# Kernel optimization log

Measured on AMD Instinct MI355X. Metric: run time of the kernel, lower is better.

The kernel has to match this reference:

```python
import jax, jax.numpy as jnp
import numpy as np

B, LAT, H, N, NL = 16, 64, 128, 256, 3
STATS = 7
IU, JU = np.triu_indices(N, 1)  # P = N*(N-1)/2 upper-triangular pairs


def _ln(x, g, b):
    m = jnp.mean(x, axis=-1, keepdims=True)
    v = jnp.var(x, axis=-1, keepdims=True)
    return (x - m) / jnp.sqrt(v + 1e-5) * g + b


def setup_inputs() -> dict:
    key = jax.random.key(0)
    ks = jax.random.split(key, 16)
    s = 0.02  # xavier-ish small gain per _init_weights
    L = NL - 1
    return {
        "x": jax.random.normal(ks[0], (B, LAT), jnp.float32),
        "stats": jax.random.normal(ks[1], (B, STATS), jnp.float32),
        # input_proj: Linear(LAT+7, 2H) + LN(2H)
        "ip_w": jax.random.normal(ks[2], (LAT + STATS, 2 * H)) * s,
        "ip_b": jnp.zeros((2 * H,)),
        "ip_ln_g": jnp.ones((2 * H,)),
        "ip_ln_b": jnp.zeros((2 * H,)),
        # dim_reduce: Linear(2H, H) + LN(H)
        "dr_w": jax.random.normal(ks[3], (2 * H, H)) * s,
        "dr_b": jnp.zeros((H,)),
        "dr_ln_g": jnp.ones((H,)),
        "dr_ln_b": jnp.zeros((H,)),
        # residual blocks (NL-1 of them), proj is Identity since in==out
        "res_lin1_w": jax.random.normal(ks[4], (L, H, H)) * s,
        "res_lin1_b": jnp.zeros((L, H)),
        "res_lin2_w": jax.random.normal(ks[5], (L, H, H)) * s,
        "res_lin2_b": jnp.zeros((L, H)),
        "res_n1_g": jnp.ones((L, H)),
        "res_n1_b": jnp.zeros((L, H)),
        "res_n2_g": jnp.ones((L, H)),
        "res_n2_b": jnp.zeros((L, H)),
        # attention: Linear(H, 1)
        "attn_w": jax.random.normal(ks[6], (H, 1)) * s,
        "attn_b": jnp.zeros((1,)),
        # edge_mlp: Linear(2H, H) + LN(H) + Linear(H, 2)
        "e1_w": jax.random.normal(ks[7], (2 * H, H)) * s,
        "e1_b": jnp.zeros((H,)),
        "e_ln_g": jnp.ones((H,)),
        "e_ln_b": jnp.zeros((H,)),
        "e2_w": jax.random.normal(ks[8], (H, 2)) * s,
        "e2_b": jnp.zeros((2,)),
        "temperature": jnp.ones((1,)) * 0.5,
    }


def reference(x, stats, ip_w, ip_b, ip_ln_g, ip_ln_b, dr_w, dr_b, dr_ln_g,
              dr_ln_b, res_lin1_w, res_lin1_b, res_lin2_w, res_lin2_b,
              res_n1_g, res_n1_b, res_n2_g, res_n2_b, attn_w, attn_b,
              e1_w, e1_b, e_ln_g, e_ln_b, e2_w, e2_b, temperature):
    # concat latent + stats, broadcast to every node: [B, N, LAT+7]
    z = jnp.concatenate([x, stats], axis=-1)
    z = jnp.broadcast_to(z[:, None, :], (B, N, LAT + STATS))
    # input_proj (dropout is identity in eval)
    h = _ln(jax.nn.relu(z @ ip_w + ip_b), ip_ln_g, ip_ln_b)
    # dim_reduce
    h = _ln(jax.nn.relu(h @ dr_w + dr_b), dr_ln_g, dr_ln_b)
    # residual blocks: h = h + 0.1 * block(h); block(h) = mlp(h) + h
    for l in range(res_lin1_w.shape[0]):
        r = _ln(h, res_n1_g[l], res_n1_b[l])
        r = jax.nn.relu(r @ res_lin1_w[l] + res_lin1_b[l])
        r = _ln(r, res_n2_g[l], res_n2_b[l])
        r = r @ res_lin2_w[l] + res_lin2_b[l]
        h = h + 0.1 * (r + h)
    # simple attention over node axis
    w = jax.nn.softmax(h @ attn_w + attn_b, axis=1)  # [B, N, 1]
    h = h * w
    # batched edge MLP over all i<j pairs: [B, P, 2H]
    edge_in = jnp.concatenate([h[:, IU], h[:, JU]], axis=-1)
    e = _ln(jax.nn.relu(edge_in @ e1_w + e1_b), e_ln_g, e_ln_b)
    logits = e @ e2_w + e2_b  # [B, P, 2]
    # gumbel-softmax (hard, straight-through), fixed key for determinism
    temp = jnp.clip(temperature, 0.1, 2.0)
    u = jax.random.uniform(jax.random.key(42), logits.shape,
                           minval=1e-9, maxval=1.0)
    gumbel = -jnp.log(-jnp.log(u))
    y = jax.nn.softmax((logits + gumbel) / temp, axis=-1)
    y_hard = jax.nn.one_hot(jnp.argmax(y, axis=-1), 2, dtype=y.dtype)
    y = y_hard + y - jax.lax.stop_gradient(y)
    xe = y[..., 0]  # [B, P]
    # scatter into upper triangle, symmetrize
    adj = jnp.zeros((B, N, N), dtype=xe.dtype).at[:, IU, JU].set(xe)
    return adj + jnp.swapaxes(adj, 1, 2)
```

## Files before the change

kernel.cpp:

```cpp
#include <hip/hip_runtime.h>
#include <stdint.h>
#include <math.h>

#define BN 16
#define LATN 64
#define STATSN 7
#define ZN 71
#define HN 128
#define H2N 256
#define NNODE 256
#define NPAIR 32640
#define NQ 522240
#define NT 1024

#define BARRIER() asm volatile("s_waitcnt lgkmcnt(0)\n\ts_barrier" ::: "memory")

__device__ __forceinline__ void tf2x32(uint32_t x0, uint32_t x1,
                                       uint32_t& o0, uint32_t& o1) {
    const uint32_t ks0 = 0u, ks1 = 42u, ks2 = 0x1BD11BF0u;
    x0 += ks0; x1 += ks1;
#define TFRND(r) { x0 += x1; x1 = (x1 << (r)) | (x1 >> (32 - (r))); x1 ^= x0; }
    TFRND(13) TFRND(15) TFRND(26) TFRND(6)
    x0 += ks1; x1 += ks2 + 1u;
    TFRND(17) TFRND(29) TFRND(16) TFRND(24)
    x0 += ks2; x1 += ks0 + 2u;
    TFRND(13) TFRND(15) TFRND(26) TFRND(6)
    x0 += ks0; x1 += ks1 + 3u;
    TFRND(17) TFRND(29) TFRND(16) TFRND(24)
    x0 += ks1; x1 += ks2 + 4u;
    TFRND(13) TFRND(15) TFRND(26) TFRND(6)
    x0 += ks2; x1 += ks0 + 5u;
#undef TFRND
    o0 = x0; o1 = x1;
}

__device__ __forceinline__ uint32_t bits_partitionable(uint32_t m) {
    uint32_t o0, o1;
    tf2x32(0u, m, o0, o1);
    return o0 ^ o1;
}

__device__ __forceinline__ float bits_to_u(uint32_t w) {
    float f = __uint_as_float((w >> 9) | 0x3f800000u) - 1.0f;
    const float mn = 1e-9f;
    return fmaxf(mn, f * (1.0f - mn) + mn);
}

template<int CTRL>
__device__ __forceinline__ double dppd(double x) {
    int lo = __double2loint(x), hi = __double2hiint(x);
    lo = __builtin_amdgcn_update_dpp(0, lo, CTRL, 0xF, 0xF, true);
    hi = __builtin_amdgcn_update_dpp(0, hi, CTRL, 0xF, 0xF, true);
    return __hiloint2double(hi, lo);
}
__device__ __forceinline__ double swz16d(double x) {
    int lo = __double2loint(x), hi = __double2hiint(x);
    lo = __builtin_amdgcn_ds_swizzle(lo, 0x401F);
    hi = __builtin_amdgcn_ds_swizzle(hi, 0x401F);
    return __hiloint2double(hi, lo);
}
__device__ __forceinline__ void bfly_pair(double& a, double& q) {
    a += dppd<0xB1>(a);   q += dppd<0xB1>(q);
    a += dppd<0x4E>(a);   q += dppd<0x4E>(q);
    a += dppd<0x141>(a);  q += dppd<0x141>(q);
    a += dppd<0x140>(a);  q += dppd<0x140>(q);
    a += swz16d(a);       q += swz16d(q);
    a += __shfl_xor(a, 32, 64);
    q += __shfl_xor(q, 32, 64);
}

template<int K, int O>
struct WS {
    static constexpr int C    = NT / O;
    static constexpr int KC   = (K + C - 1) / C;
    static constexpr int LOGO = (O == 256) ? 8 : 7;
    float w[KC];
    __device__ __forceinline__ void load(const float* __restrict__ W, int t) {
        const int out = t & (O - 1);
        const int k0 = (t >> LOGO) * KC;
#pragma unroll
        for (int i = 0; i < KC; ++i) {
            const int k = k0 + i;
            w[i] = ((K % C == 0) || k < K) ? W[k * O + out] : 0.0f;
        }
    }
    __device__ __forceinline__ double dot(const double* __restrict__ vin, int t) const {
        const int k0 = (t >> LOGO) * KC;
        double a0 = 0.0, a1 = 0.0;
#pragma unroll
        for (int i = 0; i < KC; i += 2) {
            a0 = fma(vin[k0 + i], (double)w[i], a0);
            if (i + 1 < KC) a1 = fma(vin[k0 + i + 1], (double)w[i + 1], a1);
        }
        return a0 + a1;
    }
    __device__ __forceinline__ double dot_mask127(const double* __restrict__ vin, int t) const {
        const int k0 = (t >> LOGO) * KC;
        double a0 = 0.0, a1 = 0.0;
#pragma unroll
        for (int i = 0; i < KC; i += 2) {
            a0 = fma(vin[(k0 + i) & 127], (double)w[i], a0);
            if (i + 1 < KC) a1 = fma(vin[(k0 + i + 1) & 127], (double)w[i + 1], a1);
        }
        return a0 + a1;
    }
};

template<int NV>
__device__ __forceinline__ void w0_stats(const float* v, double& m, double& rs) {
    double a = 0.0, q = 0.0;
#pragma unroll
    for (int i = 0; i < NV; ++i) {
        a += (double)v[i];
        q += (double)v[i] * (double)v[i];
    }
    bfly_pair(a, q);
    constexpr double O = (double)(NV * 64);
    m = a * (1.0 / O);
    const double d = q * (1.0 / O) - m * m + 1e-5;
    double r = (double)rsqrtf((float)d);
    r = r * (1.5 - 0.5 * d * r * r);
    r = r * (1.5 - 0.5 * d * r * r);
    rs = r;
}

#define P_IPB   0
#define P_IPG   256
#define P_IPBB  512
#define P_DRB   768
#define P_DRG   896
#define P_DRBB  1024
#define P_R1B   1152
#define P_N1G   1408
#define P_N1B   1664
#define P_N2G   1920
#define P_N2B   2176
#define P_R2B   2432
#define P_E1B   2688
#define P_EG    2816
#define P_EB    2944
#define P_E2W   3072
#define P_E2B   3328
#define P_SIZE  3332

__global__ __launch_bounds__(NT, 1) void logits_kernel(
    const float* __restrict__ x, const float* __restrict__ st,
    const float* __restrict__ ipw, const float* __restrict__ ipb,
    const float* __restrict__ ipg, const float* __restrict__ ipbb,
    const float* __restrict__ drw, const float* __restrict__ drb,
    const float* __restrict__ drg, const float* __restrict__ drbb,
    const float* __restrict__ r1w, const float* __restrict__ r1b,
    const float* __restrict__ r2w, const float* __restrict__ r2b,
    const float* __restrict__ n1g, const float* __restrict__ n1b,
    const float* __restrict__ n2g, const float* __restrict__ n2b,
    const float* __restrict__ e1w, const float* __restrict__ e1b,
    const float* __restrict__ eg,  const float* __restrict__ eb,
    const float* __restrict__ e2w, const float* __restrict__ e2b,
    float* __restrict__ out_logits)
{
    __shared__ __align__(16) double V0[H2N];
    __shared__ __align__(16) double V1[H2N];
    __shared__ double dpart[NT];
    __shared__ float P[P_SIZE];
    const int t = threadIdx.x;
    const int b = blockIdx.x;
    const int l = t & 63;
    const bool w0 = (t < 64);

    WS<ZN, H2N> w_ip;
    WS<H2N, HN> w_dr;
    WS<HN, HN>  w_r1a, w_r2a, w_r1b, w_r2b;
    WS<H2N, HN> w_e1;

    w_ip.load(ipw, t);
    w_dr.load(drw, t);
    if (t < 256) {
        P[P_IPB + t] = ipb[t];  P[P_IPG + t] = ipg[t];  P[P_IPBB + t] = ipbb[t];
        P[P_R1B + t] = r1b[t];  P[P_N1G + t] = n1g[t];  P[P_N1B + t] = n1b[t];
        P[P_N2G + t] = n2g[t];  P[P_N2B + t] = n2b[t];  P[P_R2B + t] = r2b[t];
        P[P_E2W + t] = e2w[t];
    } else if (t < 384) {
        const int i = t - 256;
        P[P_DRB + i] = drb[i];  P[P_DRG + i] = drg[i];  P[P_DRBB + i] = drbb[i];
        P[P_E1B + i] = e1b[i];  P[P_EG + i] = eg[i];    P[P_EB + i] = eb[i];
    } else if (t < 386) {
        P[P_E2B + (t - 384)] = e2b[t - 384];
    }
    if (t < LATN)      V0[t] = (double)x[b * LATN + t];
    else if (t < ZN)   V0[t] = (double)st[b * STATSN + (t - LATN)];
    else if (t < H2N)  V0[t] = 0.0;
    BARRIER();

    float h0 = 0.0f, h1 = 0.0f;

    dpart[t] = w_ip.dot(V0, t);
    BARRIER();
    w_r1a.load(r1w, t);
    if (w0) {
        float v[4];
#pragma unroll
        for (int i = 0; i < 4; ++i) {
            const int o = l + 64 * i;
            double ca = 0.0;
#pragma unroll
            for (int cc = 0; cc < 4; ++cc) ca += dpart[o + cc * H2N];
            v[i] = fmaxf((float)ca + P[P_IPB + o], 0.0f);
        }
        double m, rs; w0_stats<4>(v, m, rs);
#pragma unroll
        for (int i = 0; i < 4; ++i) {
            const int o = l + 64 * i;
            V1[o] = (double)((float)(((double)v[i] - m) * rs) * P[P_IPG + o] + P[P_IPBB + o]);
        }
    }
    BARRIER();

    dpart[t] = w_dr.dot(V1, t);
    BARRIER();
    w_r2a.load(r2w, t);
    if (w0) {
        float v[2];
#pragma unroll
        for (int i = 0; i < 2; ++i) {
            const int o = l + 64 * i;
            double ca = 0.0;
#pragma unroll
            for (int cc = 0; cc < 8; ++cc) ca += dpart[o + cc * HN];
            v[i] = fmaxf((float)ca + P[P_DRB + o], 0.0f);
        }
        double m, rs; w0_stats<2>(v, m, rs);
        h0 = (float)(((double)v[0] - m) * rs) * P[P_DRG + l] + P[P_DRBB + l];
        h1 = (float)(((double)v[1] - m) * rs) * P[P_DRG + l + 64] + P[P_DRBB + l + 64];
        float hv[2] = {h0, h1};
        double m1, rs1; w0_stats<2>(hv, m1, rs1);
        V1[l]      = (double)((float)(((double)h0 - m1) * rs1) * P[P_N1G + l] + P[P_N1B + l]);
        V1[l + 64] = (double)((float)(((double)h1 - m1) * rs1) * P[P_N1G + l + 64] + P[P_N1B + l + 64]);
    }
    BARRIER();

    dpart[t] = w_r1a.dot(V1, t);
    BARRIER();
    w_r1b.load(r1w + HN * HN, t);
    if (w0) {
        float v[2];
#pragma unroll
        for (int i = 0; i < 2; ++i) {
            const int o = l + 64 * i;
            double ca = 0.0;
#pragma unroll
            for (int cc = 0; cc < 8; ++cc) ca += dpart[o + cc * HN];
            v[i] = fmaxf((float)ca + P[P_R1B + o], 0.0f);
        }
        double m, rs; w0_stats<2>(v, m, rs);
        V1[l]      = (double)((float)(((double)v[0] - m) * rs) * P[P_N2G + l] + P[P_N2B + l]);
        V1[l + 64] = (double)((float)(((double)v[1] - m) * rs) * P[P_N2G + l + 64] + P[P_N2B + l + 64]);
    }
    BARRIER();

    dpart[t] = w_r2a.dot(V1, t);
    BARRIER();
    w_r2b.load(r2w + HN * HN, t);
    if (w0) {
        float r2o[2];
#pragma unroll
        for (int i = 0; i < 2; ++i) {
            const int o = l + 64 * i;
            double ca = 0.0;
#pragma unroll
            for (int cc = 0; cc < 8; ++cc) ca += dpart[o + cc * HN];
            r2o[i] = (float)ca + P[P_R2B + o];
        }
        h0 = h0 + 0.1f * (r2o[0] + h0);
        h1 = h1 + 0.1f * (r2o[1] + h1);
        float hv[2] = {h0, h1};
        double m1, rs1; w0_stats<2>(hv, m1, rs1);
        V1[l]      = (double)((float)(((double)h0 - m1) * rs1) * P[P_N1G + HN + l] + P[P_N1B + HN + l]);
        V1[l + 64] = (double)((float)(((double)h1 - m1) * rs1) * P[P_N1G + HN + l + 64] + P[P_N1B + HN + l + 64]);
    }
    BARRIER();

    dpart[t] = w_r1b.dot(V1, t);
    BARRIER();
    w_e1.load(e1w, t);
    if (w0) {
        float v[2];
#pragma unroll
        for (int i = 0; i < 2; ++i) {
            const int o = l + 64 * i;
            double ca = 0.0;
#pragma unroll
            for (int cc = 0; cc < 8; ++cc) ca += dpart[o + cc * HN];
            v[i] = fmaxf((float)ca + P[P_R1B + HN + o], 0.0f);
        }
        double m, rs; w0_stats<2>(v, m, rs);
        V1[l]      = (double)((float)(((double)v[0] - m) * rs) * P[P_N2G + HN + l] + P[P_N2B + HN + l]);
        V1[l + 64] = (double)((float)(((double)v[1] - m) * rs) * P[P_N2G + HN + l + 64] + P[P_N2B + HN + l + 64]);
    }
    BARRIER();

    dpart[t] = w_r2b.dot(V1, t);
    BARRIER();
    if (w0) {
        float r2o[2];
#pragma unroll
        for (int i = 0; i < 2; ++i) {
            const int o = l + 64 * i;
            double ca = 0.0;
#pragma unroll
            for (int cc = 0; cc < 8; ++cc) ca += dpart[o + cc * HN];
            r2o[i] = (float)ca + P[P_R2B + HN + o];
        }
        h0 = h0 + 0.1f * (r2o[0] + h0);
        h1 = h1 + 0.1f * (r2o[1] + h1);
        V0[l]      = (double)h0;
        V0[l + 64] = (double)h1;
    }
    BARRIER();

    dpart[t] = w_e1.dot_mask127(V0, t) * 0.00390625;
    BARRIER();
    if (w0) {
        float v[2];
#pragma unroll
        for (int i = 0; i < 2; ++i) {
            const int o = l + 64 * i;
            double ca = 0.0;
#pragma unroll
            for (int cc = 0; cc < 8; ++cc) ca += dpart[o + cc * HN];
            v[i] = fmaxf((float)ca + P[P_E1B + o], 0.0f);
        }
        double m, rs; w0_stats<2>(v, m, rs);
        const float eo0 = (float)(((double)v[0] - m) * rs) * P[P_EG + l] + P[P_EB + l];
        const float eo1 = (float)(((double)v[1] - m) * rs) * P[P_EG + l + 64] + P[P_EB + l + 64];
        double p0 = (double)eo0 * (double)P[P_E2W + 2 * l];
        p0 = fma((double)eo1, (double)P[P_E2W + 2 * (l + 64)], p0);
        double p1 = (double)eo0 * (double)P[P_E2W + 2 * l + 1];
        p1 = fma((double)eo1, (double)P[P_E2W + 2 * (l + 64) + 1], p1);
        bfly_pair(p0, p1);
        if (l == 0) {
            out_logits[b * 2]     = (float)p0 + P[P_E2B];
            out_logits[b * 2 + 1] = (float)p1 + P[P_E2B + 1];
        }
    }
}

__device__ __forceinline__ int rowbase(int i) { return (i * (2 * NNODE - 1 - i)) >> 1; }

__global__ __launch_bounds__(256) void edges_kernel(const float* __restrict__ lg,
                                                    const float* __restrict__ tptr,
                                                    float* __restrict__ out)
{
    int q = blockIdx.x * blockDim.x + threadIdx.x;
    if (q >= NQ) return;
    if (q < BN * NNODE) {
        int bb = q >> 8, ii = q & 255;
        out[(bb << 16) | (ii << 8) | ii] = 0.0f;
    }
    float temp = fminf(fmaxf(tptr[0], 0.1f), 2.0f);

    int b = q / NPAIR;
    int p = q - b * NPAIR;
    float discf = 261121.0f - 8.0f * (float)p;
    int i = (int)((511.0f - sqrtf(discf)) * 0.5f);
    if (i < 0) i = 0;
    if (i > NNODE - 2) i = NNODE - 2;
    while (rowbase(i + 1) <= p) ++i;
    while (rowbase(i) > p) --i;
    int j = p - rowbase(i) + i + 1;

    uint32_t w0 = bits_partitionable((uint32_t)(2 * q));
    uint32_t w1 = bits_partitionable((uint32_t)(2 * q + 1));

    float u0 = bits_to_u(w0), u1 = bits_to_u(w1);
    float g0 = -logf(-logf(u0));
    float g1 = -logf(-logf(u1));
    float l0 = lg[2 * b], l1 = lg[2 * b + 1];
    float A0 = (l0 + g0) / temp, A1 = (l1 + g1) / temp;
    float mx = fmaxf(A0, A1);
    float e0 = expf(A0 - mx), e1 = expf(A1 - mx);
    float ssum = e0 + e1;
    float y0 = e0 / ssum, y1 = e1 / ssum;
    float xe = (y0 >= y1) ? 1.0f : 0.0f;
    out[(b << 16) | (i << 8) | j] = xe;
    out[(b << 16) | (j << 8) | i] = xe;
}

extern "C" void kernel_launch(void* const* d_in, const int* in_sizes, int n_in,
                              void* d_out, int out_size, void* d_ws, size_t ws_size,
                              hipStream_t stream)
{
    const float* x    = (const float*)d_in[0];
    const float* st   = (const float*)d_in[1];
    const float* ipw  = (const float*)d_in[2];
    const float* ipb  = (const float*)d_in[3];
    const float* ipg  = (const float*)d_in[4];
    const float* ipbb = (const float*)d_in[5];
    const float* drw  = (const float*)d_in[6];
    const float* drb  = (const float*)d_in[7];
    const float* drg  = (const float*)d_in[8];
    const float* drbb = (const float*)d_in[9];
    const float* r1w  = (const float*)d_in[10];
    const float* r1b  = (const float*)d_in[11];
    const float* r2w  = (const float*)d_in[12];
    const float* r2b  = (const float*)d_in[13];
    const float* n1g  = (const float*)d_in[14];
    const float* n1b  = (const float*)d_in[15];
    const float* n2g  = (const float*)d_in[16];
    const float* n2b  = (const float*)d_in[17];
    const float* e1w  = (const float*)d_in[20];
    const float* e1b  = (const float*)d_in[21];
    const float* eg   = (const float*)d_in[22];
    const float* eb   = (const float*)d_in[23];
    const float* e2w  = (const float*)d_in[24];
    const float* e2b  = (const float*)d_in[25];
    const float* temp = (const float*)d_in[26];
    float* out = (float*)d_out;
    float* lg  = (float*)d_ws;

    hipLaunchKernelGGL(logits_kernel, dim3(BN), dim3(NT), 0, stream,
        x, st, ipw, ipb, ipg, ipbb, drw, drb, drg, drbb,
        r1w, r1b, r2w, r2b, n1g, n1b, n2g, n2b,
        e1w, e1b, eg, eb, e2w, e2b, lg);
    hipLaunchKernelGGL(edges_kernel, dim3((NQ + 255) / 256), dim3(256), 0, stream,
        lg, temp, out);
}
```

Before: 23.15 us.

## Halve barriers by having every wave redundantly compute the per-layer reduction

Drops the wave-0-only epilogue, so all 16 waves redundantly reduce the partial dot products and apply layernorm themselves. Each wave then writes identical vector values and runs the next matvec with only a local LDS wait, removing one block barrier per layer. Partial-sum buffers now alternate between two arrays so a fast wave cannot overwrite partials that a slower wave is still reading. The cost is redundant LDS reads and ALU work in every wave, plus races where several waves write the same V1 entries with the same values.

```diff
diff --git a/kernel.cpp b/kernel.cpp
--- a/kernel.cpp
+++ b/kernel.cpp
@@ -14,6 +14,7 @@
 #define NT 1024
 
 #define BARRIER() asm volatile("s_waitcnt lgkmcnt(0)\n\ts_barrier" ::: "memory")
+#define LGKM0()   asm volatile("s_waitcnt lgkmcnt(0)" ::: "memory")
 
 __device__ __forceinline__ void tf2x32(uint32_t x0, uint32_t x1,
                                        uint32_t& o0, uint32_t& o1) {
@@ -107,7 +108,7 @@
 };
 
 template<int NV>
-__device__ __forceinline__ void w0_stats(const float* v, double& m, double& rs) {
+__device__ __forceinline__ void w_stats(const float* v, double& m, double& rs) {
     double a = 0.0, q = 0.0;
 #pragma unroll
     for (int i = 0; i < NV; ++i) {
@@ -160,12 +161,12 @@
 {
     __shared__ __align__(16) double V0[H2N];
     __shared__ __align__(16) double V1[H2N];
-    __shared__ double dpart[NT];
+    __shared__ double dpA[NT];
+    __shared__ double dpB[NT];
     __shared__ float P[P_SIZE];
     const int t = threadIdx.x;
     const int b = blockIdx.x;
     const int l = t & 63;
-    const bool w0 = (t < 64);
 
     WS<ZN, H2N> w_ip;
     WS<H2N, HN> w_dr;
@@ -193,121 +194,122 @@
 
     float h0 = 0.0f, h1 = 0.0f;
 
-    dpart[t] = w_ip.dot(V0, t);
-    BARRIER();
+    dpA[t] = w_ip.dot(V0, t);
     w_r1a.load(r1w, t);
-    if (w0) {
+    BARRIER();
+
+    {
         float v[4];
 #pragma unroll
         for (int i = 0; i < 4; ++i) {
             const int o = l + 64 * i;
             double ca = 0.0;
 #pragma unroll
-            for (int cc = 0; cc < 4; ++cc) ca += dpart[o + cc * H2N];
+            for (int cc = 0; cc < 4; ++cc) ca += dpA[o + cc * H2N];
             v[i] = fmaxf((float)ca + P[P_IPB + o], 0.0f);
         }
-        double m, rs; w0_stats<4>(v, m, rs);
+        double m, rs; w_stats<4>(v, m, rs);
 #pragma unroll
         for (int i = 0; i < 4; ++i) {
             const int o = l + 64 * i;
             V1[o] = (double)((float)(((double)v[i] - m) * rs) * P[P_IPG + o] + P[P_IPBB + o]);
         }
     }
-    BARRIER();
-
-    dpart[t] = w_dr.dot(V1, t);
-    BARRIER();
+    LGKM0();
+    dpB[t] = w_dr.dot(V1, t);
     w_r2a.load(r2w, t);
-    if (w0) {
+    BARRIER();
+
+    {
         float v[2];
 #pragma unroll
         for (int i = 0; i < 2; ++i) {
             const int o = l + 64 * i;
             double ca = 0.0;
 #pragma unroll
-            for (int cc = 0; cc < 8; ++cc) ca += dpart[o + cc * HN];
+            for (int cc = 0; cc < 8; ++cc) ca += dpB[o + cc * HN];
             v[i] = fmaxf((float)ca + P[P_DRB + o], 0.0f);
         }
-        double m, rs; w0_stats<2>(v, m, rs);
+        double m, rs; w_stats<2>(v, m, rs);
         h0 = (float)(((double)v[0] - m) * rs) * P[P_DRG + l] + P[P_DRBB + l];
         h1 = (float)(((double)v[1] - m) * rs) * P[P_DRG + l + 64] + P[P_DRBB + l + 64];
         float hv[2] = {h0, h1};
-        double m1, rs1; w0_stats<2>(hv, m1, rs1);
+        double m1, rs1; w_stats<2>(hv, m1, rs1);
         V1[l]      = (double)((float)(((double)h0 - m1) * rs1) * P[P_N1G + l] + P[P_N1B + l]);
         V1[l + 64] = (double)((float)(((double)h1 - m1) * rs1) * P[P_N1G + l + 64] + P[P_N1B + l + 64]);
     }
-    BARRIER();
-
-    dpart[t] = w_r1a.dot(V1, t);
-    BARRIER();
+    LGKM0();
+    dpA[t] = w_r1a.dot(V1, t);
     w_r1b.load(r1w + HN * HN, t);
-    if (w0) {
+    BARRIER();
+
+    {
         float v[2];
 #pragma unroll
         for (int i = 0; i < 2; ++i) {
             const int o = l + 64 * i;
             double ca = 0.0;
 #pragma unroll
-            for (int cc = 0; cc < 8; ++cc) ca += dpart[o + cc * HN];
+            for (int cc = 0; cc < 8; ++cc) ca += dpA[o + cc * HN];
             v[i] = fmaxf((float)ca + P[P_R1B + o], 0.0f);
         }
-        double m, rs; w0_stats<2>(v, m, rs);
+        double m, rs; w_stats<2>(v, m, rs);
         V1[l]      = (double)((float)(((double)v[0] - m) * rs) * P[P_N2G + l] + P[P_N2B + l]);
         V1[l + 64] = (double)((float)(((double)v[1] - m) * rs) * P[P_N2G + l + 64] + P[P_N2B + l + 64]);
     }
-    BARRIER();
-
-    dpart[t] = w_r2a.dot(V1, t);
-    BARRIER();
+    LGKM0();
+    dpB[t] = w_r2a.dot(V1, t);
     w_r2b.load(r2w + HN * HN, t);
-    if (w0) {
+    BARRIER();
+
+    {
         float r2o[2];
 #pragma unroll
         for (int i = 0; i < 2; ++i) {
             const int o = l + 64 * i;
             double ca = 0.0;
 #pragma unroll
-            for (int cc = 0; cc < 8; ++cc) ca += dpart[o + cc * HN];
+            for (int cc = 0; cc < 8; ++cc) ca += dpB[o + cc * HN];
             r2o[i] = (float)ca + P[P_R2B + o];
         }
         h0 = h0 + 0.1f * (r2o[0] + h0);
         h1 = h1 + 0.1f * (r2o[1] + h1);
         float hv[2] = {h0, h1};
-        double m1, rs1; w0_stats<2>(hv, m1, rs1);
+        double m1, rs1; w_stats<2>(hv, m1, rs1);
         V1[l]      = (double)((float)(((double)h0 - m1) * rs1) * P[P_N1G + HN + l] + P[P_N1B + HN + l]);
         V1[l + 64] = (double)((float)(((double)h1 - m1) * rs1) * P[P_N1G + HN + l + 64] + P[P_N1B + HN + l + 64]);
     }
-    BARRIER();
-
-    dpart[t] = w_r1b.dot(V1, t);
-    BARRIER();
+    LGKM0();
+    dpA[t] = w_r1b.dot(V1, t);
     w_e1.load(e1w, t);
-    if (w0) {
+    BARRIER();
+
+    {
         float v[2];
 #pragma unroll
         for (int i = 0; i < 2; ++i) {
             const int o = l + 64 * i;
             double ca = 0.0;
 #pragma unroll
-            for (int cc = 0; cc < 8; ++cc) ca += dpart[o + cc * HN];
+            for (int cc = 0; cc < 8; ++cc) ca += dpA[o + cc * HN];
             v[i] = fmaxf((float)ca + P[P_R1B + HN + o], 0.0f);
         }
-        double m, rs; w0_stats<2>(v, m, rs);
+        double m, rs; w_stats<2>(v, m, rs);
         V1[l]      = (double)((float)(((double)v[0] - m) * rs) * P[P_N2G + HN + l] + P[P_N2B + HN + l]);
         V1[l + 64] = (double)((float)(((double)v[1] - m) * rs) * P[P_N2G + HN + l + 64] + P[P_N2B + HN + l + 64]);
     }
-    BARRIER();
-
-    dpart[t] = w_r2b.dot(V1, t);
-    BARRIER();
-    if (w0) {
+    LGKM0();
+    dpB[t] = w_r2b.dot(V1, t);
+    BARRIER();
+
+    {
         float r2o[2];
 #pragma unroll
         for (int i = 0; i < 2; ++i) {
             const int o = l + 64 * i;
             double ca = 0.0;
 #pragma unroll
-            for (int cc = 0; cc < 8; ++cc) ca += dpart[o + cc * HN];
+            for (int cc = 0; cc < 8; ++cc) ca += dpB[o + cc * HN];
             r2o[i] = (float)ca + P[P_R2B + HN + o];
         }
         h0 = h0 + 0.1f * (r2o[0] + h0);
@@ -315,21 +317,21 @@
         V0[l]      = (double)h0;
         V0[l + 64] = (double)h1;
     }
-    BARRIER();
-
-    dpart[t] = w_e1.dot_mask127(V0, t) * 0.00390625;
-    BARRIER();
-    if (w0) {
+    LGKM0();
+    dpA[t] = w_e1.dot_mask127(V0, t) * 0.00390625;
+    BARRIER();
+
+    {
         float v[2];
 #pragma unroll
         for (int i = 0; i < 2; ++i) {
             const int o = l + 64 * i;
             double ca = 0.0;
 #pragma unroll
-            for (int cc = 0; cc < 8; ++cc) ca += dpart[o + cc * HN];
+            for (int cc = 0; cc < 8; ++cc) ca += dpA[o + cc * HN];
             v[i] = fmaxf((float)ca + P[P_E1B + o], 0.0f);
         }
-        double m, rs; w0_stats<2>(v, m, rs);
+        double m, rs; w_stats<2>(v, m, rs);
         const float eo0 = (float)(((double)v[0] - m) * rs) * P[P_EG + l] + P[P_EB + l];
         const float eo1 = (float)(((double)v[1] - m) * rs) * P[P_EG + l + 64] + P[P_EB + l + 64];
         double p0 = (double)eo0 * (double)P[P_E2W + 2 * l];
@@ -337,7 +339,7 @@
         double p1 = (double)eo0 * (double)P[P_E2W + 2 * l + 1];
         p1 = fma((double)eo1, (double)P[P_E2W + 2 * (l + 64) + 1], p1);
         bfly_pair(p0, p1);
-        if (l == 0) {
+        if (t == 0) {
             out_logits[b * 2]     = (float)p0 + P[P_E2B];
             out_logits[b * 2 + 1] = (float)p1 + P[P_E2B + 1];
         }
```

Result: slower. 27.33 us (+18.1%).

## Overlap Gumbel noise generation with logits kernel using extra idle blocks

Applied to the files above, without the earlier changes.

Adds extra blocks to the logits kernel launch. They compute the Threefry-based Gumbel noise for all pairs and store it in workspace, running alongside the 16 MLP blocks that otherwise leave most CUs idle. The edges kernel then only reads the precomputed noise, applies the softmax decision and scatters. The cost is an extra ~4MB write and read through global memory, and the path depends on the workspace being large enough.

```diff
diff --git a/kernel.cpp b/kernel.cpp
--- a/kernel.cpp
+++ b/kernel.cpp
@@ -12,6 +12,7 @@
 #define NPAIR 32640
 #define NQ 522240
 #define NT 1024
+#define GBLK 128
 
 #define BARRIER() asm volatile("s_waitcnt lgkmcnt(0)\n\ts_barrier" ::: "memory")
 
@@ -156,7 +157,7 @@
     const float* __restrict__ e1w, const float* __restrict__ e1b,
     const float* __restrict__ eg,  const float* __restrict__ eb,
     const float* __restrict__ e2w, const float* __restrict__ e2b,
-    float* __restrict__ out_logits)
+    float* __restrict__ out_logits, float2* __restrict__ gum)
 {
     __shared__ __align__(16) double V0[H2N];
     __shared__ __align__(16) double V1[H2N];
@@ -164,6 +165,19 @@
     __shared__ float P[P_SIZE];
     const int t = threadIdx.x;
     const int b = blockIdx.x;
+
+    if (b >= BN) {
+        const int gid = (b - BN) * NT + t;
+        for (int q = gid; q < NQ; q += GBLK * NT) {
+            const uint32_t w0b = bits_partitionable((uint32_t)(2 * q));
+            const uint32_t w1b = bits_partitionable((uint32_t)(2 * q + 1));
+            const float g0 = -logf(-logf(bits_to_u(w0b)));
+            const float g1 = -logf(-logf(bits_to_u(w1b)));
+            gum[q] = make_float2(g0, g1);
+        }
+        return;
+    }
+
     const int l = t & 63;
     const bool w0 = (t < 64);
 
@@ -346,6 +360,47 @@
 
 __device__ __forceinline__ int rowbase(int i) { return (i * (2 * NNODE - 1 - i)) >> 1; }
 
+__device__ __forceinline__ void decide_scatter(int q, float g0, float g1,
+                                               const float* __restrict__ lg,
+                                               float temp, float* __restrict__ out)
+{
+    int b = q / NPAIR;
+    int p = q - b * NPAIR;
+    float discf = 261121.0f - 8.0f * (float)p;
+    int i = (int)((511.0f - sqrtf(discf)) * 0.5f);
+    if (i < 0) i = 0;
+    if (i > NNODE - 2) i = NNODE - 2;
+    while (rowbase(i + 1) <= p) ++i;
+    while (rowbase(i) > p) --i;
+    int j = p - rowbase(i) + i + 1;
+
+    float l0 = lg[2 * b], l1 = lg[2 * b + 1];
+    float A0 = (l0 + g0) / temp, A1 = (l1 + g1) / temp;
+    float mx = fmaxf(A0, A1);
+    float e0 = expf(A0 - mx), e1 = expf(A1 - mx);
+    float ssum = e0 + e1;
+    float y0 = e0 / ssum, y1 = e1 / ssum;
+    float xe = (y0 >= y1) ? 1.0f : 0.0f;
+    out[(b << 16) | (i << 8) | j] = xe;
+    out[(b << 16) | (j << 8) | i] = xe;
+}
+
+__global__ __launch_bounds__(256) void edges_final(const float* __restrict__ lg,
+                                                   const float* __restrict__ tptr,
+                                                   const float2* __restrict__ gum,
+                                                   float* __restrict__ out)
+{
+    int q = blockIdx.x * blockDim.x + threadIdx.x;
+    if (q >= NQ) return;
+    if (q < BN * NNODE) {
+        int bb = q >> 8, ii = q & 255;
+        out[(bb << 16) | (ii << 8) | ii] = 0.0f;
+    }
+    float temp = fminf(fmaxf(tptr[0], 0.1f), 2.0f);
+    const float2 g = gum[q];
+    decide_scatter(q, g.x, g.y, lg, temp, out);
+}
+
 __global__ __launch_bounds__(256) void edges_kernel(const float* __restrict__ lg,
                                                     const float* __restrict__ tptr,
                                                     float* __restrict__ out)
@@ -357,32 +412,11 @@
         out[(bb << 16) | (ii << 8) | ii] = 0.0f;
     }
     float temp = fminf(fmaxf(tptr[0], 0.1f), 2.0f);
-
-    int b = q / NPAIR;
-    int p = q - b * NPAIR;
-    float discf = 261121.0f - 8.0f * (float)p;
-    int i = (int)((511.0f - sqrtf(discf)) * 0.5f);
-    if (i < 0) i = 0;
-    if (i > NNODE - 2) i = NNODE - 2;
-    while (rowbase(i + 1) <= p) ++i;
-    while (rowbase(i) > p) --i;
-    int j = p - rowbase(i) + i + 1;
-
     uint32_t w0 = bits_partitionable((uint32_t)(2 * q));
     uint32_t w1 = bits_partitionable((uint32_t)(2 * q + 1));
-
-    float u0 = bits_to_u(w0), u1 = bits_to_u(w1);
-    float g0 = -logf(-logf(u0));
-    float g1 = -logf(-logf(u1));
-    float l0 = lg[2 * b], l1 = lg[2 * b + 1];
-    float A0 = (l0 + g0) / temp, A1 = (l1 + g1) / temp;
-    float mx = fmaxf(A0, A1);
-    float e0 = expf(A0 - mx), e1 = expf(A1 - mx);
-    float ssum = e0 + e1;
-    float y0 = e0 / ssum, y1 = e1 / ssum;
-    float xe = (y0 >= y1) ? 1.0f : 0.0f;
-    out[(b << 16) | (i << 8) | j] = xe;
-    out[(b << 16) | (j << 8) | i] = xe;
+    float g0 = -logf(-logf(bits_to_u(w0)));
+    float g1 = -logf(-logf(bits_to_u(w1)));
+    decide_scatter(q, g0, g1, lg, temp, out);
 }
 
 extern "C" void kernel_launch(void* const* d_in, const int* in_sizes, int n_in,
@@ -416,11 +450,20 @@
     const float* temp = (const float*)d_in[26];
     float* out = (float*)d_out;
     float* lg  = (float*)d_ws;
-
-    hipLaunchKernelGGL(logits_kernel, dim3(BN), dim3(NT), 0, stream,
+    float2* gum = (float2*)((char*)d_ws + 256);
+
+    const size_t need = 256 + (size_t)NQ * sizeof(float2);
+    const bool split = (ws_size >= need);
+
+    hipLaunchKernelGGL(logits_kernel, dim3(split ? BN + GBLK : BN), dim3(NT), 0, stream,
         x, st, ipw, ipb, ipg, ipbb, drw, drb, drg, drbb,
         r1w, r1b, r2w, r2b, n1g, n1b, n2g, n2b,
-        e1w, e1b, eg, eb, e2w, e2b, lg);
-    hipLaunchKernelGGL(edges_kernel, dim3((NQ + 255) / 256), dim3(256), 0, stream,
-        lg, temp, out);
-}
+        e1w, e1b, eg, eb, e2w, e2b, lg, gum);
+    if (split) {
+        hipLaunchKernelGGL(edges_final, dim3((NQ + 255) / 256), dim3(256), 0, stream,
+            lg, temp, gum, out);
+    } else {
+        hipLaunchKernelGGL(edges_kernel, dim3((NQ + 255) / 256), dim3(256), 0, stream,
+            lg, temp, out);
+    }
+}
```

Result: slower. 24.71 us (+6.7%).
